# Optimization experiments

Hardware: AMD Instinct MI355X
Metric: run time of the kernel (lower is better)

Reference implementation:

```python
import jax, jax.numpy as jnp
import numpy as np

B, L, C = 8, 999, 768
C2 = C // 2           # 384 per branch
H, HD = 8, C2 // 8    # heads, head_dim=48
K, G = 3, 2           # dynamic conv kernel size, num_groups
DC_IN = C2 // 4       # DynamicConv1d proj inner (reduction_ratio default 4) = 96
PJ_IN = max(16, C // 8)  # mixer proj inner_dim = 96
SCALE = HD ** -0.5
EPS = 1e-5


def _gelu(x):
    return jax.nn.gelu(x, approximate=False)


def _c1x1(x, w, b):
    # pointwise conv1d: x (B,Cin,L), w (Cout,Cin), b (Cout,)
    return jnp.einsum('bcl,oc->bol', x, w) + b[None, :, None]


def _dw3(x, w, b):
    # depthwise conv1d k=3 pad=1: x (B,Ch,L), w (Ch,3), b (Ch,) or None
    Lx = x.shape[-1]
    xp = jnp.pad(x, ((0, 0), (0, 0), (1, 1)))
    y = (xp[:, :, 0:Lx] * w[:, 0][None, :, None]
         + xp[:, :, 1:Lx + 1] * w[:, 1][None, :, None]
         + xp[:, :, 2:Lx + 2] * w[:, 2][None, :, None])
    if b is not None:
        y = y + b[None, :, None]
    return y


def _bn(x, g, b):
    # BatchNorm1d, training-mode batch stats over (B, L): x (B,Ch,L)
    m = x.mean(axis=(0, 2), keepdims=True)
    v = ((x - m) ** 2).mean(axis=(0, 2), keepdims=True)
    return (x - m) * jax.lax.rsqrt(v + EPS) * g[None, :, None] + b[None, :, None]


def setup_inputs() -> dict:
    key = jax.random.key(0)
    ks = jax.random.split(key, 30)
    s = 0.02
    d = {
        'x': jax.random.normal(ks[0], (B, L, C), jnp.float32),
        # DynamicConv1d (dim=384, K=3, G=2, inner=96)
        'dc_weight': jax.random.normal(ks[1], (G, C2, K), jnp.float32) * s,
        'dc_bias':   jax.random.normal(ks[2], (G, C2), jnp.float32) * s,
        'dc_p1w':    jax.random.normal(ks[3], (DC_IN, C2), jnp.float32) * s,
        'dc_p1b':    jax.random.normal(ks[4], (DC_IN,), jnp.float32) * s,
        'dc_p2w':    jax.random.normal(ks[5], (C2 * G, DC_IN), jnp.float32) * s,
        'dc_p2b':    jax.random.normal(ks[6], (C2 * G,), jnp.float32) * s,
        # Attention (dim=384, heads=8, sr_ratio=1 -> sr=Identity)
        'at_qw':  jax.random.normal(ks[7], (C2, C2), jnp.float32) * s,
        'at_qb':  jax.random.normal(ks[8], (C2,), jnp.float32) * s,
        'at_kvw': jax.random.normal(ks[9], (2 * C2, C2), jnp.float32) * s,
        'at_kvb': jax.random.normal(ks[10], (2 * C2,), jnp.float32) * s,
        'at_lcw': jax.random.normal(ks[11], (C2, K), jnp.float32) * s,
        'at_lcb': jax.random.normal(ks[12], (C2,), jnp.float32) * s,
        # mixer proj
        'pj_dww':  jax.random.normal(ks[13], (C, K), jnp.float32) * s,
        'pj_dwb':  jax.random.normal(ks[14], (C,), jnp.float32) * s,
        'pj_bn1g': jnp.ones((C,), jnp.float32),
        'pj_bn1b': jnp.zeros((C,), jnp.float32),
        'pj_c1w':  jax.random.normal(ks[15], (PJ_IN, C), jnp.float32) * s,
        'pj_c1b':  jax.random.normal(ks[16], (PJ_IN,), jnp.float32) * s,
        'pj_bn2g': jnp.ones((PJ_IN,), jnp.float32),
        'pj_bn2b': jnp.zeros((PJ_IN,), jnp.float32),
        'pj_c2w':  jax.random.normal(ks[17], (C, PJ_IN), jnp.float32) * s,
        'pj_c2b':  jax.random.normal(ks[18], (C,), jnp.float32) * s,
        'pj_bn3g': jnp.ones((C,), jnp.float32),
        'pj_bn3b': jnp.zeros((C,), jnp.float32),
    }
    return d


def _dynamic_conv(x, dc_weight, dc_bias, p1w, p1b, p2w, p2b):
    # x: (B, L, C2)
    xt = jnp.transpose(x, (0, 2, 1))                 # (B,C2,L)
    # AdaptiveAvgPool1d(K) with L divisible by K -> exact non-overlapping mean
    pooled = xt.reshape(B, C2, K, L // K).mean(-1)   # (B,C2,K)
    sc = _c1x1(_gelu(_c1x1(pooled, p1w, p1b)), p2w, p2b)  # (B, G*C2, K)
    sc = jax.nn.softmax(sc.reshape(B, G, C2, K), axis=1)
    w = (sc * dc_weight[None]).sum(axis=1)           # (B,C2,K) per-sample kernels
    xm = xt.mean(axis=2, keepdims=True)              # (B,C2,1)
    sb = _c1x1(_gelu(_c1x1(xm, p1w, p1b)), p2w, p2b) # (B, G*C2, 1)
    sb = jax.nn.softmax(sb.reshape(B, G, C2), axis=1)
    bias = (sb * dc_bias[None]).sum(axis=1)          # (B,C2)
    # depthwise per-(b,c) conv, k=3, pad=1
    xp = jnp.pad(xt, ((0, 0), (0, 0), (1, 1)))
    y = (xp[:, :, 0:L] * w[:, :, 0:1]
         + xp[:, :, 1:L + 1] * w[:, :, 1:2]
         + xp[:, :, 2:L + 2] * w[:, :, 2:3]) + bias[:, :, None]
    return jnp.transpose(y, (0, 2, 1))               # (B,L,C2)


def _attention(x, qw, qb, kvw, kvb, lcw, lcb):
    # x: (B, L, C2)
    xt = jnp.transpose(x, (0, 2, 1))                 # (B,C2,L)
    q = _c1x1(xt, qw, qb).reshape(B, H, HD, L)
    q = jnp.transpose(q, (0, 1, 3, 2))               # (B,H,L,HD)
    kv_in = _dw3(xt, lcw, lcb) + xt                  # local_conv(kv)+kv (sr=Identity)
    kv = _c1x1(kv_in, kvw, kvb)                      # (B,2*C2,L)
    k = kv[:, :C2].reshape(B, H, HD, L)              # (B,H,HD,L)
    v = jnp.transpose(kv[:, C2:].reshape(B, H, HD, L), (0, 1, 3, 2))  # (B,H,L,HD)
    attn = jnp.einsum('bhld,bhdm->bhlm', q, k) * SCALE
    attn = jax.nn.softmax(attn, axis=-1)
    out = jnp.einsum('bhlm,bhmd->bhld', attn, v)     # (B,H,L,HD)
    # faithful to torch: transpose(-1,-2) then reshape(B, L, C2)
    out = jnp.transpose(out, (0, 1, 3, 2)).reshape(B, L, C2)
    return out


def reference(x, dc_weight, dc_bias, dc_p1w, dc_p1b, dc_p2w, dc_p2b,
              at_qw, at_qb, at_kvw, at_kvb, at_lcw, at_lcb,
              pj_dww, pj_dwb, pj_bn1g, pj_bn1b, pj_c1w, pj_c1b,
              pj_bn2g, pj_bn2b, pj_c2w, pj_c2b, pj_bn3g, pj_bn3b):
    x1 = x[:, :, :C2]
    x2 = x[:, :, C2:]
    x1 = _dynamic_conv(x1, dc_weight, dc_bias, dc_p1w, dc_p1b, dc_p2w, dc_p2b)
    x2 = _attention(x2, at_qw, at_qb, at_kvw, at_kvb, at_lcw, at_lcb)
    xc = jnp.concatenate([x1, x2], axis=2)           # (B,L,C)
    xt = jnp.transpose(xc, (0, 2, 1))                # (B,C,L)
    h = _bn(_gelu(_dw3(xt, pj_dww, pj_dwb)), pj_bn1g, pj_bn1b)
    h = _bn(_gelu(_c1x1(h, pj_c1w, pj_c1b)), pj_bn2g, pj_bn2b)
    h = _bn(_c1x1(h, pj_c2w, pj_c2b), pj_bn3g, pj_bn3b)
    out = h + xt
    return jnp.transpose(out, (0, 2, 1))             # (B,L,C)
```

## Files before the change

### kernel.cpp

```cpp
#include <hip/hip_runtime.h>
#include <cstddef>

constexpr int B = 8, L = 999, C = 768, C2 = 384, H = 8, HD = 48;
constexpr int KVL = 1000;
constexpr float ATT_SCALE = 0.14433756729740644f;
constexpr float LOG2E = 1.4426950408889634f;
constexpr float BN_EPS = 1e-5f;
constexpr float INV_N = 1.0f / (8.0f * 999.0f);

constexpr size_t SZ_XT   = (size_t)B * C * L;
constexpr size_t SZ_HALF = (size_t)B * C2 * L;
constexpr size_t OFF_XT  = 0;
constexpr size_t OFF_XT2 = SZ_XT;
constexpr size_t OFF_KV  = 2 * SZ_XT;
constexpr size_t OFF_AX  = 3 * SZ_XT;
constexpr size_t OFF_Q   = 3 * SZ_XT + SZ_HALF;
constexpr size_t OFF_SM  = 3 * SZ_XT + SZ_HALF + SZ_HALF / 2;

constexpr size_t SM_POOLED = 0;
constexpr size_t SM_XM     = 9216;
constexpr size_t SM_H1     = 12288;
constexpr size_t SM_WDYN   = 15360;
constexpr size_t SM_BDYN   = 24576;
constexpr size_t SM_SUM1   = 27648;
constexpr size_t SM_SQ1    = 28416;
constexpr size_t SM_S1     = 29184;
constexpr size_t SM_M1     = 29952;
constexpr size_t SM_CB1    = 30720;
constexpr size_t SM_SUM2   = 30816;
constexpr size_t SM_SQ2    = 30912;
constexpr size_t SM_S2     = 31008;
constexpr size_t SM_M2     = 31104;
constexpr size_t SM_CB2    = 31200;
constexpr size_t SM_SUM3   = 31968;
constexpr size_t SM_SQ3    = 32736;
constexpr size_t SM_S3     = 33504;
constexpr size_t SM_D3     = 34272;
constexpr size_t SM_END    = 35040;
constexpr size_t SM_WQ  = SM_END;
constexpr size_t SM_WKV = SM_WQ + 73728;
constexpr size_t SM_WC1 = SM_WKV + 147456;
constexpr size_t SM_WC2 = SM_WC1 + 36864;

typedef __attribute__((ext_vector_type(8))) short bf16x8;
typedef __attribute__((ext_vector_type(4))) float floatx4;

__device__ __forceinline__ float gelu_f(float x) {
  return 0.5f * x * (1.0f + erff(x * 0.70710678118654752f));
}

__device__ __forceinline__ float wave_sum(float v) {
  #pragma unroll
  for (int off = 32; off > 0; off >>= 1) v += __shfl_down(v, off, 64);
  return v;
}

__device__ __forceinline__ short f2bf(float f) {
  union { float f; unsigned u; } x; x.f = f;
  unsigned r = x.u + 0x7FFFu + ((x.u >> 16) & 1u);
  return (short)(r >> 16);
}

__device__ __forceinline__ bf16x8 pack8(const float* p) {
  union { unsigned u[4]; bf16x8 v; } r;
  asm("v_cvt_pk_bf16_f32 %0, %1, %2" : "=v"(r.u[0]) : "v"(p[0]), "v"(p[1]));
  asm("v_cvt_pk_bf16_f32 %0, %1, %2" : "=v"(r.u[1]) : "v"(p[2]), "v"(p[3]));
  asm("v_cvt_pk_bf16_f32 %0, %1, %2" : "=v"(r.u[2]) : "v"(p[4]), "v"(p[5]));
  asm("v_cvt_pk_bf16_f32 %0, %1, %2" : "=v"(r.u[3]) : "v"(p[6]), "v"(p[7]));
  return r.v;
}

__device__ __forceinline__ float exp2_hw(float x) {
  float r;
  asm("v_exp_f32 %0, %1" : "=v"(r) : "v"(x));
  return r;
}

__global__ void k_prep(const float* __restrict__ qw, short* __restrict__ wq,
                       const float* __restrict__ kvw, short* __restrict__ wkv,
                       const float* __restrict__ c1w, short* __restrict__ wc1,
                       const float* __restrict__ c2w, short* __restrict__ wc2,
                       const float* __restrict__ c1b, const float* __restrict__ bn1b,
                       const float* __restrict__ c2b, const float* __restrict__ bn2b,
                       float* __restrict__ cb1, float* __restrict__ cb2) {
  int bid = blockIdx.x;
  if (bid < 288) {
    const float* src; short* dst; int base;
    if (bid < 72)       { src = qw;  dst = wq;  base = bid; }
    else if (bid < 216) { src = kvw; dst = wkv; base = bid - 72; }
    else if (bid < 252) { src = c1w; dst = wc1; base = bid - 216; }
    else                { src = c2w; dst = wc2; base = bid - 252; }
    int i = (base * 256 + threadIdx.x) * 8;
    float4 a = *reinterpret_cast<const float4*>(&src[i]);
    float4 b = *reinterpret_cast<const float4*>(&src[i + 4]);
    short tmp[8] = {f2bf(a.x), f2bf(a.y), f2bf(a.z), f2bf(a.w),
                    f2bf(b.x), f2bf(b.y), f2bf(b.z), f2bf(b.w)};
    *(bf16x8*)&dst[i] = *(bf16x8*)tmp;
  } else if (bid == 288) {
    int o = threadIdx.x;
    if (o < 96) {
      float a = c1b[o];
      const float* wr = c1w + (size_t)o * C;
      for (int c = 0; c < C; c++) a += bn1b[c] * wr[c];
      cb1[o] = a;
    }
  } else {
    for (int o = threadIdx.x; o < C; o += 256) {
      float a = c2b[o];
      const float* wr = c2w + (size_t)o * 96;
      for (int i = 0; i < 96; i++) a += bn2b[i] * wr[i];
      cb2[o] = a;
    }
  }
}

__global__ __launch_bounds__(384) void k_kvin(const float* __restrict__ x,
                                              const float* __restrict__ lcw,
                                              const float* __restrict__ lcb,
                                              short* __restrict__ x2bf,
                                              short* __restrict__ kvinbf) {
  int b = blockIdx.y, l0 = blockIdx.x * 8, c = threadIdx.x;
  float w0 = lcw[c * 3], w1 = lcw[c * 3 + 1] + 1.0f, w2 = lcw[c * 3 + 2], bb = lcb[c];
  const float* xb = x + (size_t)b * L * C + C2 + c;
  float prev = (l0 > 0) ? xb[(size_t)(l0 - 1) * C] : 0.f;
  float cur  = (l0 < L) ? xb[(size_t)l0 * C] : 0.f;
  #pragma unroll
  for (int r = 0; r < 8; r++) {
    int l = l0 + r;
    if (l >= L) break;
    float nxt = (l + 1 < L) ? xb[(size_t)(l + 1) * C] : 0.f;
    x2bf[((size_t)b * L + l) * C2 + c]   = f2bf(cur);
    kvinbf[((size_t)b * L + l) * C2 + c] = f2bf(prev * w0 + cur * w1 + nxt * w2 + bb);
    prev = cur; cur = nxt;
  }
}

__global__ void k_transpose_in(const float* __restrict__ x, float* __restrict__ xt) {
  __shared__ float tile[32][33];
  int b = blockIdx.z;
  int l0 = blockIdx.x * 32, c0 = blockIdx.y * 32;
  int tx = threadIdx.x, ty = threadIdx.y;
  #pragma unroll
  for (int i = 0; i < 4; i++) {
    int l = l0 + ty + i * 8, c = c0 + tx;
    if (l < L) tile[ty + i * 8][tx] = x[((size_t)b * L + l) * C + c];
  }
  __syncthreads();
  #pragma unroll
  for (int i = 0; i < 4; i++) {
    int c = c0 + ty + i * 8, l = l0 + tx;
    if (l < L) xt[((size_t)b * C + c) * L + l] = tile[tx][ty + i * 8];
  }
}

__global__ __launch_bounds__(256) void k_pool(const float* __restrict__ xt,
                                              float* __restrict__ pooled,
                                              float* __restrict__ xm) {
  int c = blockIdx.x, b = blockIdx.y;
  const float* row = xt + ((size_t)b * C + c) * L;
  float s0 = 0.f, s1 = 0.f, s2 = 0.f;
  for (int l = threadIdx.x; l < L; l += 256) {
    float v = row[l];
    int ch = l / 333;
    if (ch == 0) s0 += v; else if (ch == 1) s1 += v; else s2 += v;
  }
  s0 = wave_sum(s0); s1 = wave_sum(s1); s2 = wave_sum(s2);
  __shared__ float r[3][4];
  int lane = threadIdx.x & 63, wid = threadIdx.x >> 6;
  if (lane == 0) { r[0][wid] = s0; r[1][wid] = s1; r[2][wid] = s2; }
  __syncthreads();
  if (threadIdx.x == 0) {
    float t0 = r[0][0] + r[0][1] + r[0][2] + r[0][3];
    float t1 = r[1][0] + r[1][1] + r[1][2] + r[1][3];
    float t2 = r[2][0] + r[2][1] + r[2][2] + r[2][3];
    size_t pb = (size_t)(b * C2 + c) * 3;
    pooled[pb + 0] = t0 / 333.f;
    pooled[pb + 1] = t1 / 333.f;
    pooled[pb + 2] = t2 / 333.f;
    xm[b * C2 + c] = (t0 + t1 + t2) / 999.f;
  }
}

__global__ void k_mlp1(const float* __restrict__ pooled, const float* __restrict__ xm,
                       const float* __restrict__ p1w, const float* __restrict__ p1b,
                       float* __restrict__ h1) {
  int j = blockIdx.x, b = blockIdx.y;
  __shared__ float vin[C2];
  for (int c = threadIdx.x; c < C2; c += 128)
    vin[c] = (j < 3) ? pooled[(size_t)(b * C2 + c) * 3 + j] : xm[b * C2 + c];
  __syncthreads();
  int o = threadIdx.x;
  if (o < 96) {
    float acc = p1b[o];
    const float* wr = p1w + (size_t)o * C2;
    for (int c = 0; c < C2; c++) acc += vin[c] * wr[c];
    h1[(b * 4 + j) * 96 + o] = gelu_f(acc);
  }
}

__global__ void k_mix2(const float* __restrict__ h1,
                       const float* __restrict__ p2w, const float* __restrict__ p2b,
                       const float* __restrict__ dcw, const float* __restrict__ dcb,
                       float* __restrict__ wdyn, float* __restrict__ bdyn) {
  int j = blockIdx.x, b = blockIdx.y;
  __shared__ float hv[96];
  for (int i = threadIdx.x; i < 96; i += 384) hv[i] = h1[(b * 4 + j) * 96 + i];
  __syncthreads();
  int c = threadIdx.x;
  float a0 = p2b[c], a1 = p2b[C2 + c];
  const float* w0r = p2w + (size_t)c * 96;
  const float* w1r = p2w + (size_t)(C2 + c) * 96;
  for (int i = 0; i < 96; i++) { float h = hv[i]; a0 += h * w0r[i]; a1 += h * w1r[i]; }
  float m = fmaxf(a0, a1);
  float e0 = __expf(a0 - m), e1 = __expf(a1 - m);
  float inv = 1.f / (e0 + e1);
  float p0 = e0 * inv, p1 = e1 * inv;
  if (j < 3)
    wdyn[(size_t)(b * C2 + c) * 3 + j] = p0 * dcw[(size_t)c * 3 + j] + p1 * dcw[(size_t)(C2 + c) * 3 + j];
  else
    bdyn[b * C2 + c] = p0 * dcb[c] + p1 * dcb[C2 + c];
}

__global__ __launch_bounds__(256) void k_dwconv(const float* __restrict__ xt,
                                                const float* __restrict__ wdyn,
                                                const float* __restrict__ bdyn,
                                                float* __restrict__ xt2) {
  int c = blockIdx.x, b = blockIdx.y;
  const float* rowA = xt + ((size_t)b * C + c) * L;
  size_t wb = (size_t)(b * C2 + c) * 3;
  float a0 = wdyn[wb], a1 = wdyn[wb + 1], a2 = wdyn[wb + 2], ab = bdyn[b * C2 + c];
  float* oA = xt2 + ((size_t)b * C + c) * L;
  for (int l = threadIdx.x; l < L; l += 256) {
    float xm1 = (l > 0) ? rowA[l - 1] : 0.f;
    float x0 = rowA[l];
    float xp1 = (l < L - 1) ? rowA[l + 1] : 0.f;
    oA[l] = xm1 * a0 + x0 * a1 + xp1 * a2 + ab;
  }
}

template<int LT, bool XBF16>
__global__ __launch_bounds__(256) void k_gemm3(const short* __restrict__ Wbf,
                                               const void* __restrict__ Xv,
                                               void* __restrict__ Yv,
                                               const float* __restrict__ shift,
                                               const float* __restrict__ scale,
                                               const float* __restrict__ bias,
                                               float* __restrict__ sum, float* __restrict__ sq,
                                               int O, int Kd, int Kstride, int XLd, int Ldy,
                                               size_t xbs, size_t ybs,
                                               int flags, float outmul,
                                               int ksplit, size_t slice) {
  __shared__ __align__(16) short Xt[2][LT * 72];
  constexpr int R = LT / 32;
  int b = blockIdx.z;
  int kc = (int)blockIdx.y % ksplit;
  int o0 = ((int)blockIdx.y / ksplit) * 64;
  int l0 = blockIdx.x * LT;
  int kbeg = kc * Kd;
  int t = threadIdx.x, w = t >> 6, lane = t & 63;
  int col = lane & 15, quad = lane >> 4;
  int KT = (Kd + 63) >> 6;

  floatx4 acc[LT / 16];
  #pragma unroll
  for (int i = 0; i < LT / 16; i++) acc[i] = floatx4{0.f, 0.f, 0.f, 0.f};

  int orow = o0 + w * 16 + col;
  bool wok = orow < O;
  const short* Wrow = Wbf + (size_t)orow * Kstride + kbeg;

  const short* Xb16 = (const short*)Xv + (size_t)b * xbs + kbeg;
  const float* Xb32 = (const float*)Xv + (size_t)b * xbs + kbeg;

  bf16x8 xr[R];
  float4 xf[R][2];
  bf16x8 wcur0, wcur1, wnxt0, wnxt1;

  auto xload = [&](int k0) {
    #pragma unroll
    for (int r = 0; r < R; r++) {
      int u = t + r * 256;
      int ll = u >> 3, oct = u & 7;
      int l = l0 + ll, kk = k0 + oct * 8;
      bool ok = (l < L) && (kk < Kd);
      if constexpr (XBF16) {
        xr[r] = ok ? *(const bf16x8*)&Xb16[(size_t)l * XLd + kk]
                   : bf16x8{0, 0, 0, 0, 0, 0, 0, 0};
      } else {
        if (ok) {
          const float* p = &Xb32[(size_t)l * XLd + kk];
          float4 a = *(const float4*)p;
          float4 bq = *(const float4*)(p + 4);
          if (shift) {
            float4 sh0 = *(const float4*)&shift[kbeg + kk];
            float4 sh1 = *(const float4*)&shift[kbeg + kk + 4];
            float4 sc0 = *(const float4*)&scale[kbeg + kk];
            float4 sc1 = *(const float4*)&scale[kbeg + kk + 4];
            a.x = (a.x - sh0.x) * sc0.x;  a.y = (a.y - sh0.y) * sc0.y;
            a.z = (a.z - sh0.z) * sc0.z;  a.w = (a.w - sh0.w) * sc0.w;
            bq.x = (bq.x - sh1.x) * sc1.x; bq.y = (bq.y - sh1.y) * sc1.y;
            bq.z = (bq.z - sh1.z) * sc1.z; bq.w = (bq.w - sh1.w) * sc1.w;
          }
          xf[r][0] = a;
          xf[r][1] = bq;
        } else {
          xf[r][0] = float4{0.f, 0.f, 0.f, 0.f};
          xf[r][1] = float4{0.f, 0.f, 0.f, 0.f};
        }
      }
    }
  };
  auto xwrite = [&](int buf) {
    #pragma unroll
    for (int r = 0; r < R; r++) {
      int u = t + r * 256;
      int ll = u >> 3, oct = u & 7;
      bf16x8 val;
      if constexpr (XBF16) {
        val = xr[r];
      } else {
        union { unsigned u4[4]; bf16x8 v; } pk;
        asm("v_cvt_pk_bf16_f32 %0, %1, %2" : "=v"(pk.u4[0]) : "v"(xf[r][0].x), "v"(xf[r][0].y));
        asm("v_cvt_pk_bf16_f32 %0, %1, %2" : "=v"(pk.u4[1]) : "v"(xf[r][0].z), "v"(xf[r][0].w));
        asm("v_cvt_pk_bf16_f32 %0, %1, %2" : "=v"(pk.u4[2]) : "v"(xf[r][1].x), "v"(xf[r][1].y));
        asm("v_cvt_pk_bf16_f32 %0, %1, %2" : "=v"(pk.u4[3]) : "v"(xf[r][1].z), "v"(xf[r][1].w));
        val = pk.v;
      }
      *(bf16x8*)&Xt[buf][ll * 72 + oct * 8] = val;
    }
  };
  auto wload = [&](int k0, bf16x8& f0, bf16x8& f1) {
    int kk0 = k0 + quad * 8;
    int kk1 = k0 + 32 + quad * 8;
    f0 = (wok && kk0 < Kd) ? *(const bf16x8*)&Wrow[kk0] : bf16x8{0, 0, 0, 0, 0, 0, 0, 0};
    f1 = (wok && kk1 < Kd) ? *(const bf16x8*)&Wrow[kk1] : bf16x8{0, 0, 0, 0, 0, 0, 0, 0};
  };

  xload(0);
  wload(0, wcur0, wcur1);
  xwrite(0);
  __syncthreads();

  for (int it = 0; it < KT; ++it) {
    int curb = it & 1;
    bool more = (it + 1 < KT);
    if (more) { xload((it + 1) * 64); wload((it + 1) * 64, wnxt0, wnxt1); }
    #pragma unroll
    for (int nt = 0; nt < LT / 16; nt++) {
      bf16x8 bx0 = *(bf16x8*)&Xt[curb][(nt * 16 + col) * 72 + quad * 8];
      acc[nt] = __builtin_amdgcn_mfma_f32_16x16x32_bf16(wcur0, bx0, acc[nt], 0, 0, 0);
      bf16x8 bx1 = *(bf16x8*)&Xt[curb][(nt * 16 + col) * 72 + 32 + quad * 8];
      acc[nt] = __builtin_amdgcn_mfma_f32_16x16x32_bf16(wcur1, bx1, acc[nt], 0, 0, 0);
    }
    if (more) xwrite(curb ^ 1);
    __syncthreads();
    wcur0 = wnxt0; wcur1 = wnxt1;
  }

  int o_base = o0 + w * 16 + quad * 4;
  #pragma unroll
  for (int r = 0; r < 4; r++) {
    int o = o_base + r;
    bool ov = o < O;
    float bo = (bias && ov) ? bias[o] : 0.f;
    float ps = 0.f, pq = 0.f;
    #pragma unroll
    for (int nt = 0; nt < LT / 16; nt++) {
      int l = l0 + nt * 16 + col;
      float v = acc[nt][r] + bo;
      if (flags & 1) v = gelu_f(v);
      v *= outmul;
      if (l >= L) v = 0.f;
      if (ov && l < L) {
        if (flags & 2) ((short*)Yv)[(size_t)b * ybs + (size_t)o * Ldy + l] = f2bf(v);
        else           ((float*)Yv)[kc * slice + (size_t)b * ybs + (size_t)o * Ldy + l] = v;
      }
      ps += v; pq += v * v;
    }
    if ((flags & 8) && ov) {
      ps += __shfl_xor(ps, 1); ps += __shfl_xor(ps, 2);
      ps += __shfl_xor(ps, 4); ps += __shfl_xor(ps, 8);
      pq += __shfl_xor(pq, 1); pq += __shfl_xor(pq, 2);
      pq += __shfl_xor(pq, 4); pq += __shfl_xor(pq, 8);
      if (col == 0) { atomicAdd(&sum[o], ps); atomicAdd(&sq[o], pq); }
    }
  }
}

__global__ __launch_bounds__(256) void k_h2fin_t(const float* __restrict__ part,
                                                 const float* __restrict__ cb1,
                                                 float* __restrict__ h2,
                                                 float* __restrict__ sum, float* __restrict__ sq) {
  __shared__ float tile[96][33];
  __shared__ float lsum[96], lsq[96];
  constexpr size_t SL = (size_t)B * 96 * L;
  int b = blockIdx.y, l0 = blockIdx.x * 32;
  int t = threadIdx.x;
  #pragma unroll
  for (int p = 0; p < 12; p++) {
    int u = t + p * 256;
    int o = u >> 5, li = u & 31;
    int l = l0 + li;
    float v = 0.f;
    if (l < L) {
      size_t idx = ((size_t)b * 96 + o) * L + l;
      v = gelu_f(part[idx] + part[SL + idx] + part[2 * SL + idx] + part[3 * SL + idx] + cb1[o]);
    }
    tile[o][li] = v;
    float vs = v, vq = v * v;
    vs += __shfl_xor(vs, 1); vs += __shfl_xor(vs, 2); vs += __shfl_xor(vs, 4);
    vs += __shfl_xor(vs, 8); vs += __shfl_xor(vs, 16);
    vq += __shfl_xor(vq, 1); vq += __shfl_xor(vq, 2); vq += __shfl_xor(vq, 4);
    vq += __shfl_xor(vq, 8); vq += __shfl_xor(vq, 16);
    if ((t & 31) == 0) { lsum[o] = vs; lsq[o] = vq; }
  }
  __syncthreads();
  if (t < 96) { atomicAdd(&sum[t], lsum[t]); atomicAdd(&sq[t], lsq[t]); }
  #pragma unroll
  for (int p = 0; p < 12; p++) {
    int u = t + p * 256;
    int lr = u / 96, o = u % 96;
    int l = l0 + lr;
    if (l < L) h2[((size_t)b * L + l) * 96 + o] = tile[o][lr];
  }
}

__global__ __launch_bounds__(512, 4) void k_attn_mfma(const short* __restrict__ q,
                                                      const short* __restrict__ kv,
                                                      float* __restrict__ out) {
  __shared__ __align__(16) char smem[2 * 8192 + 2 * 6144 + 33280];
  short* Ks0 = (short*)smem;
  short* Ks1 = (short*)(smem + 8192);
  short* Vf0 = (short*)(smem + 16384);
  short* Vf1 = (short*)(smem + 22528);
  float* PF  = (float*)(smem + 28672);
  float* Os  = (float*)smem;

  int lt0 = blockIdx.x * 128;
  int h = blockIdx.y, b = blockIdx.z;
  int t = threadIdx.x;
  int w = t >> 6, lane = t & 63;
  int col = lane & 15, quad = lane >> 4;
  const short* qb = q  + ((size_t)b * C2 + h * HD) * L;
  const short* kb = kv + ((size_t)b * C  + h * HD) * KVL;
  const short* vb = kv + ((size_t)b * C + C2 + h * HD) * KVL;

  bf16x8 aq0, aq1;
  {
    int l = lt0 + w * 16 + col;
    bool ok = l < L;
    const short* qp = qb + (size_t)(quad * 8) * L + l;
    short v0[8];
    #pragma unroll
    for (int jj = 0; jj < 8; jj++) v0[jj] = ok ? qp[(size_t)jj * L] : (short)0;
    aq0 = *(bf16x8*)v0;
    if (quad < 2) {
      const short* qp1 = qb + (size_t)(32 + quad * 8) * L + l;
      short v1[8];
      #pragma unroll
      for (int jj = 0; jj < 8; jj++) v1[jj] = ok ? qp1[(size_t)jj * L] : (short)0;
      aq1 = *(bf16x8*)v1;
    } else {
      aq1 = bf16x8{0, 0, 0, 0, 0, 0, 0, 0};
    }
  }

  short kreg[8];
  bf16x8 vreg;

  auto stage_load = [&](int m0) {
    if (t < 384) {
      int m = t & 63, j = t >> 6;
      int gm = m0 + m;
      bool ok = gm < L;
      const short* src = kb + (size_t)(8 * j) * KVL + gm;
      #pragma unroll
      for (int jj = 0; jj < 8; jj++) kreg[jj] = ok ? src[(size_t)jj * KVL] : (short)0;
    }
    if (t >= 128) {
      int a = t - 128;
      int d = (a & 7) | ((a >> 6) << 3);
      int o = (a >> 3) & 7;
      int mb = m0 + o * 8;
      const short* src = vb + (size_t)d * KVL + mb;
      if (mb + 8 <= L) {
        vreg = *(const bf16x8*)src;
      } else {
        short tmp[8];
        #pragma unroll
        for (int j = 0; j < 8; j++) tmp[j] = (mb + j < L) ? src[j] : (short)0;
        vreg = *(bf16x8*)tmp;
      }
    }
  };
  auto stage_write = [&](short* Kd, short* Vd) {
    if (t < 384) {
      int m = t & 63, j = t >> 6;
      int slot = ((m >> 4) * 2 + (j >> 2)) * 64 + (j & 3) * 16 + (m & 15);
      *(bf16x8*)&Kd[slot * 8] = *(bf16x8*)kreg;
    }
    if (t >= 128) {
      int a = t - 128;
      int d = (a & 7) | ((a >> 6) << 3);
      int o = (a >> 3) & 7;
      int lanep = ((o & 3) << 4) | (d & 15);
      *(bf16x8*)&Vd[(((o >> 2) * 3 + (d >> 4)) * 64 + lanep) * 8] = vreg;
    }
  };

  if (t < 256) {
    int i = t & 127;
    int ms = i >> 5, qq = 2 + ((i >> 4) & 1), cc = i & 15;
    int slot = (ms * 2 + 1) * 64 + qq * 16 + cc;
    short* Kd = (t < 128) ? Ks0 : Ks1;
    *(bf16x8*)&Kd[slot * 8] = bf16x8{0, 0, 0, 0, 0, 0, 0, 0};
  }

  stage_load(0);
  stage_write(Ks0, Vf0);

  floatx4 of[3];
  #pragma unroll
  for (int i = 0; i < 3; i++) of[i] = floatx4{0.f, 0.f, 0.f, 0.f};
  float rs[4] = {0.f, 0.f, 0.f, 0.f};
  __syncthreads();

  for (int it = 0; it < 16; ++it) {
    int m0 = it * 64;
    short* Kc = (it & 1) ? Ks1 : Ks0;
    short* Vc = (it & 1) ? Vf1 : Vf0;
    short* Kn = (it & 1) ? Ks0 : Ks1;
    short* Vn = (it & 1) ? Vf0 : Vf1;
    if (it < 15) stage_load(m0 + 64);

    floatx4 sf[4];
    __builtin_amdgcn_s_setprio(1);
    #pragma unroll
    for (int ms = 0; ms < 4; ms++) {
      bf16x8 bk0 = *(bf16x8*)&Kc[((ms * 2 + 0) * 64 + lane) * 8];
      bf16x8 bk1 = *(bf16x8*)&Kc[((ms * 2 + 1) * 64 + lane) * 8];
      floatx4 a4 = floatx4{0.f, 0.f, 0.f, 0.f};
      a4 = __builtin_amdgcn_mfma_f32_16x16x32_bf16(aq0, bk0, a4, 0, 0, 0);
      a4 = __builtin_amdgcn_mfma_f32_16x16x32_bf16(aq1, bk1, a4, 0, 0, 0);
      sf[ms] = a4;
    }
    __builtin_amdgcn_s_setprio(0);

    float* pw = PF + w * 1040 + lane;
    #pragma unroll
    for (int ms = 0; ms < 4; ms++) {
      int m = m0 + ms * 16 + col;
      bool ok = m < L;
      #pragma unroll
      for (int r = 0; r < 4; r++) {
        float e = ok ? exp2_hw(sf[ms][r]) : 0.f;
        rs[r] += e;
        pw[(ms * 4 + r) * 65] = e;
      }
    }

    const float* pr = PF + w * 1040 + (col & 3) * 65 + (col >> 2) * 16 + (quad & 1) * 8;
    __builtin_amdgcn_s_setprio(1);
    #pragma unroll
    for (int mh = 0; mh < 2; mh++) {
      const float* ps = pr + (mh * 2 + (quad >> 1)) * 260;
      float p8[8];
      #pragma unroll
      for (int jj = 0; jj < 8; jj++) p8[jj] = ps[jj];
      bf16x8 ap = pack8(p8);
      #pragma unroll
      for (int ds = 0; ds < 3; ds++) {
        bf16x8 bv = *(bf16x8*)&Vc[((mh * 3 + ds) * 64 + lane) * 8];
        of[ds] = __builtin_amdgcn_mfma_f32_16x16x32_bf16(ap, bv, of[ds], 0, 0, 0);
      }
    }
    __builtin_amdgcn_s_setprio(0);
    if (it < 15) stage_write(Kn, Vn);
    __syncthreads();
  }

  #pragma unroll
  for (int r = 0; r < 4; r++) {
    float v = rs[r];
    v += __shfl_xor(v, 1); v += __shfl_xor(v, 2);
    v += __shfl_xor(v, 4); v += __shfl_xor(v, 8);
    rs[r] = v;
  }
  #pragma unroll
  for (int r = 0; r < 4; r++) {
    float inv = 1.f / rs[r];
    #pragma unroll
    for (int ds = 0; ds < 3; ds++)
      Os[(ds * 16 + col) * 130 + w * 16 + quad * 4 + r] = of[ds][r] * inv;
  }
  __syncthreads();
  for (int i = t; i < 48 * 128; i += 512) {
    int d = i >> 7, ll = i & 127;
    int l = lt0 + ll;
    if (l < L) out[((size_t)b * C2 + h * HD + d) * L + l] = Os[d * 130 + ll];
  }
}

__global__ void k_fill_xt2(const float* __restrict__ ao, float* __restrict__ xt2) {
  __shared__ float tile[32][33];
  int b = blockIdx.z;
  int l0 = blockIdx.x * 32, c0 = blockIdx.y * 32;
  int tx = threadIdx.x, ty = threadIdx.y;
  #pragma unroll
  for (int i = 0; i < 4; i++) {
    int l = l0 + ty + i * 8, c = c0 + tx;
    if (l < L) tile[ty + i * 8][tx] = ao[(size_t)b * ((size_t)L * C2) + (size_t)l * C2 + c];
  }
  __syncthreads();
  #pragma unroll
  for (int i = 0; i < 4; i++) {
    int c = c0 + ty + i * 8, l = l0 + tx;
    if (l < L) xt2[((size_t)b * C + C2 + c) * L + l] = tile[tx][ty + i * 8];
  }
}

__global__ __launch_bounds__(256) void k_dwproj_t(const float* __restrict__ xt2,
                                                  const float* __restrict__ dww,
                                                  const float* __restrict__ dwb,
                                                  float* __restrict__ t1,
                                                  float* __restrict__ sum, float* __restrict__ sq) {
  __shared__ float tile[32][67];
  __shared__ float rs[4][32], rq[4][32];
  int b = blockIdx.z, c0 = blockIdx.y * 32, l0 = blockIdx.x * 64;
  int t = threadIdx.x;
  for (int u = t; u < 32 * 66; u += 256) {
    int cc = u / 66, li = u % 66;
    int l = l0 - 1 + li;
    tile[cc][li] = (l >= 0 && l < L) ? xt2[((size_t)b * C + c0 + cc) * L + l] : 0.f;
  }
  __syncthreads();
  int c = c0 + (t & 31);
  float w0 = dww[c * 3], w1 = dww[c * 3 + 1], w2 = dww[c * 3 + 2], bb = dwb[c];
  int cc = t & 31;
  float s = 0.f, s2 = 0.f;
  #pragma unroll
  for (int p = 0; p < 8; p++) {
    int lr = (t >> 5) + p * 8;
    int l = l0 + lr;
    float v = 0.f;
    if (l < L) {
      v = gelu_f(tile[cc][lr] * w0 + tile[cc][lr + 1] * w1 + tile[cc][lr + 2] * w2 + bb);
      t1[((size_t)b * L + l) * C + c] = v;
    }
    s += v; s2 += v * v;
  }
  s += __shfl_xor(s, 32, 64); s2 += __shfl_xor(s2, 32, 64);
  int wv = t >> 6, ln = t & 63;
  if (ln < 32) { rs[wv][ln] = s; rq[wv][ln] = s2; }
  __syncthreads();
  if (t < 32) {
    float a = rs[0][t] + rs[1][t] + rs[2][t] + rs[3][t];
    float qq = rq[0][t] + rq[1][t] + rq[2][t] + rq[3][t];
    atomicAdd(&sum[c0 + t], a);
    atomicAdd(&sq[c0 + t], qq);
  }
}

__global__ void k_bnfin(const float* __restrict__ sum, const float* __restrict__ sq,
                        const float* __restrict__ g, int n,
                        float* __restrict__ s_, float* __restrict__ m_) {
  int t = threadIdx.x;
  if (t < n) {
    float m = sum[t] * INV_N;
    float v = sq[t] * INV_N - m * m;
    float r = rsqrtf(v + BN_EPS);
    s_[t] = g[t] * r;
    m_[t] = m;
  }
}

__global__ void k_fin3(const float* __restrict__ sum, const float* __restrict__ sq,
                       const float* __restrict__ g, const float* __restrict__ be,
                       float* __restrict__ s3, float* __restrict__ d3) {
  int t = threadIdx.x;
  if (t < C) {
    float m = sum[t] * INV_N;
    float v = sq[t] * INV_N - m * m;
    float r = rsqrtf(v + BN_EPS);
    float sc = g[t] * r;
    s3[t] = sc;
    d3[t] = be[t] - m * sc;
  }
}

__global__ void k_final(const float* __restrict__ y3, const float* __restrict__ xt2,
                        const float* __restrict__ s3, const float* __restrict__ d3,
                        float* __restrict__ out) {
  __shared__ float tile[32][33];
  int b = blockIdx.z;
  int l0 = blockIdx.x * 32, c0 = blockIdx.y * 32;
  int tx = threadIdx.x, ty = threadIdx.y;
  #pragma unroll
  for (int i = 0; i < 4; i++) {
    int c = c0 + ty + i * 8, l = l0 + tx;
    if (l < L) {
      size_t idx = ((size_t)b * C + c) * L + l;
      tile[ty + i * 8][tx] = y3[idx] * s3[c] + d3[c] + xt2[idx];
    }
  }
  __syncthreads();
  #pragma unroll
  for (int i = 0; i < 4; i++) {
    int l = l0 + ty + i * 8, c = c0 + tx;
    if (l < L) out[((size_t)b * L + l) * C + c] = tile[tx][ty + i * 8];
  }
}

extern "C" void kernel_launch(void* const* d_in, const int* in_sizes, int n_in,
                              void* d_out, int out_size, void* d_ws, size_t ws_size,
                              hipStream_t stream) {
  const float* x    = (const float*)d_in[0];
  const float* dcw  = (const float*)d_in[1];
  const float* dcb  = (const float*)d_in[2];
  const float* p1w  = (const float*)d_in[3];
  const float* p1b  = (const float*)d_in[4];
  const float* p2w  = (const float*)d_in[5];
  const float* p2b  = (const float*)d_in[6];
  const float* qw   = (const float*)d_in[7];
  const float* qb   = (const float*)d_in[8];
  const float* kvw  = (const float*)d_in[9];
  const float* kvb  = (const float*)d_in[10];
  const float* lcw  = (const float*)d_in[11];
  const float* lcb  = (const float*)d_in[12];
  const float* dww  = (const float*)d_in[13];
  const float* dwb  = (const float*)d_in[14];
  const float* bn1g = (const float*)d_in[15];
  const float* bn1b = (const float*)d_in[16];
  const float* c1w  = (const float*)d_in[17];
  const float* c1b  = (const float*)d_in[18];
  const float* bn2g = (const float*)d_in[19];
  const float* bn2b = (const float*)d_in[20];
  const float* c2w  = (const float*)d_in[21];
  const float* c2b  = (const float*)d_in[22];
  const float* bn3g = (const float*)d_in[23];
  const float* bn3b = (const float*)d_in[24];
  float* out = (float*)d_out;
  float* ws  = (float*)d_ws;

  float* xt      = ws + OFF_XT;
  float* xt2     = ws + OFF_XT2;
  short* kvbuf   = (short*)(ws + OFF_KV);
  float* y3      = ws + OFF_KV;
  short* x2bf    = (short*)(ws + OFF_AX);
  short* kvinbf  = (short*)(ws + OFF_AX + SZ_HALF / 2);
  float* attnout = ws + OFF_AX;
  float* c1part  = ws + OFF_AX;
  short* qbuf    = (short*)(ws + OFF_Q);
  float* h2      = ws + OFF_Q;
  float* sm      = ws + OFF_SM;

  float* pooled = sm + SM_POOLED;
  float* xm     = sm + SM_XM;
  float* h1     = sm + SM_H1;
  float* wdyn   = sm + SM_WDYN;
  float* bdyn   = sm + SM_BDYN;
  float* sum1 = sm + SM_SUM1; float* sq1 = sm + SM_SQ1;
  float* s1 = sm + SM_S1; float* m1 = sm + SM_M1; float* cb1 = sm + SM_CB1;
  float* sum2 = sm + SM_SUM2; float* sq2 = sm + SM_SQ2;
  float* s2 = sm + SM_S2; float* m2 = sm + SM_M2; float* cb2 = sm + SM_CB2;
  float* sum3 = sm + SM_SUM3; float* sq3 = sm + SM_SQ3;
  float* s3 = sm + SM_S3; float* d3 = sm + SM_D3;
  short* wqbf  = (short*)(sm + SM_WQ);
  short* wkvbf = (short*)(sm + SM_WKV);
  short* wc1bf = (short*)(sm + SM_WC1);
  short* wc2bf = (short*)(sm + SM_WC2);

  hipMemsetAsync((void*)(sm + SM_SUM1), 0, (SM_S3 - SM_SUM1) * sizeof(float), stream);

  k_prep<<<290, 256, 0, stream>>>(qw, wqbf, kvw, wkvbf, c1w, wc1bf, c2w, wc2bf,
                                  c1b, bn1b, c2b, bn2b, cb1, cb2);
  k_kvin<<<dim3(125, B), 384, 0, stream>>>(x, lcw, lcb, x2bf, kvinbf);

  dim3 tb32(32, 8);
  k_transpose_in<<<dim3(32, 12, B), tb32, 0, stream>>>(x, xt);
  k_pool<<<dim3(C2, B), 256, 0, stream>>>(xt, pooled, xm);
  k_mlp1<<<dim3(4, B), 128, 0, stream>>>(pooled, xm, p1w, p1b, h1);
  k_mix2<<<dim3(4, B), 384, 0, stream>>>(h1, p2w, p2b, dcw, dcb, wdyn, bdyn);
  k_dwconv<<<dim3(C2, B), 256, 0, stream>>>(xt, wdyn, bdyn, xt2);
  k_gemm3<64, true><<<dim3(16, 6, B), 256, 0, stream>>>(
      wqbf, (const void*)x2bf, (void*)qbuf, nullptr, nullptr, qb, nullptr, nullptr,
      C2, C2, C2, C2, L, (size_t)C2 * L, (size_t)C2 * L, 2, ATT_SCALE * LOG2E, 1, 0);
  k_gemm3<128, true><<<dim3(8, 12, B), 256, 0, stream>>>(
      wkvbf, (const void*)kvinbf, (void*)kvbuf, nullptr, nullptr, kvb, nullptr, nullptr,
      C, C2, C2, C2, KVL, (size_t)C2 * L, (size_t)C * KVL, 2, 1.0f, 1, 0);
  k_attn_mfma<<<dim3(8, H, B), 512, 0, stream>>>(qbuf, kvbuf, attnout);
  k_fill_xt2<<<dim3(32, 12, B), tb32, 0, stream>>>(attnout, xt2);
  k_dwproj_t<<<dim3(16, 24, B), 256, 0, stream>>>(xt2, dww, dwb, xt, sum1, sq1);
  k_bnfin<<<1, 768, 0, stream>>>(sum1, sq1, bn1g, C, s1, m1);
  k_gemm3<128, false><<<dim3(8, 8, B), 256, 0, stream>>>(
      wc1bf, (const void*)xt, (void*)c1part, m1, s1, nullptr, nullptr, nullptr,
      96, 192, C, C, L, (size_t)C * L, (size_t)96 * L, 0, 1.0f, 4, (size_t)B * 96 * L);
  k_h2fin_t<<<dim3(32, B), 256, 0, stream>>>(c1part, cb1, h2, sum2, sq2);
  k_bnfin<<<1, 768, 0, stream>>>(sum2, sq2, bn2g, 96, s2, m2);
  k_gemm3<128, false><<<dim3(8, 12, B), 256, 0, stream>>>(
      wc2bf, (const void*)h2, (void*)y3, m2, s2, cb2, sum3, sq3,
      C, 96, 96, 96, L, (size_t)96 * L, (size_t)C * L, 8, 1.0f, 1, 0);
  k_fin3<<<1, 768, 0, stream>>>(sum3, sq3, bn3g, bn3b, s3, d3);
  k_final<<<dim3(32, 24, B), tb32, 0, stream>>>(y3, xt2, s3, d3, out);
}
```

Before: 354.7 us.

## Fuse small kernels: merge Q/KV GEMMs, inline BN finalize, drop transpose passes

Merges the input transpose into the weight-prep kernel and the Q and KV projection GEMMs into one launch. It deletes the BN-finalize kernels by computing mean and scale from the sums inside the consuming GEMM loaders and the final kernel. It also removes the attention-output transpose into xt2, so the depthwise-projection and final kernels read the attention output directly in (B,L,C2) layout. Together these cut launch count and one full transpose round trip through memory. The cost is redundant rsqrt and BN math per element in the GEMM X-loads and the final kernel, a strided gather for half the channels in the dwproj tile load, and a larger 128-wide L tile for the Q GEMM.

```diff
diff --git a/kernel.cpp b/kernel.cpp
--- a/kernel.cpp
+++ b/kernel.cpp
@@ -24,18 +24,13 @@
 constexpr size_t SM_BDYN   = 24576;
 constexpr size_t SM_SUM1   = 27648;
 constexpr size_t SM_SQ1    = 28416;
-constexpr size_t SM_S1     = 29184;
-constexpr size_t SM_M1     = 29952;
 constexpr size_t SM_CB1    = 30720;
 constexpr size_t SM_SUM2   = 30816;
 constexpr size_t SM_SQ2    = 30912;
-constexpr size_t SM_S2     = 31008;
-constexpr size_t SM_M2     = 31104;
 constexpr size_t SM_CB2    = 31200;
 constexpr size_t SM_SUM3   = 31968;
 constexpr size_t SM_SQ3    = 32736;
-constexpr size_t SM_S3     = 33504;
-constexpr size_t SM_D3     = 34272;
+constexpr size_t SM_ZEND   = 33504;
 constexpr size_t SM_END    = 35040;
 constexpr size_t SM_WQ  = SM_END;
 constexpr size_t SM_WKV = SM_WQ + 73728;
@@ -76,40 +71,61 @@
   return r;
 }
 
-__global__ void k_prep(const float* __restrict__ qw, short* __restrict__ wq,
-                       const float* __restrict__ kvw, short* __restrict__ wkv,
-                       const float* __restrict__ c1w, short* __restrict__ wc1,
-                       const float* __restrict__ c2w, short* __restrict__ wc2,
-                       const float* __restrict__ c1b, const float* __restrict__ bn1b,
-                       const float* __restrict__ c2b, const float* __restrict__ bn2b,
-                       float* __restrict__ cb1, float* __restrict__ cb2) {
+#define BNA(x, su, qq, gg) { float m_ = (su) * INV_N; float v_ = (qq) * INV_N - m_ * m_; \
+  float sc_ = (gg) * rsqrtf(v_ + BN_EPS); (x) = ((x) - m_) * sc_; }
+
+__global__ void k_pre_t(const float* __restrict__ qw, short* __restrict__ wq,
+                        const float* __restrict__ kvw, short* __restrict__ wkv,
+                        const float* __restrict__ c1w, short* __restrict__ wc1,
+                        const float* __restrict__ c2w, short* __restrict__ wc2,
+                        const float* __restrict__ c1b, const float* __restrict__ bn1b,
+                        const float* __restrict__ c2b, const float* __restrict__ bn2b,
+                        float* __restrict__ cb1, float* __restrict__ cb2,
+                        const float* __restrict__ x, float* __restrict__ xt) {
+  __shared__ float tile[32][33];
   int bid = blockIdx.x;
+  int t = threadIdx.y * 32 + threadIdx.x;
   if (bid < 288) {
     const float* src; short* dst; int base;
     if (bid < 72)       { src = qw;  dst = wq;  base = bid; }
     else if (bid < 216) { src = kvw; dst = wkv; base = bid - 72; }
     else if (bid < 252) { src = c1w; dst = wc1; base = bid - 216; }
     else                { src = c2w; dst = wc2; base = bid - 252; }
-    int i = (base * 256 + threadIdx.x) * 8;
+    int i = (base * 256 + t) * 8;
     float4 a = *reinterpret_cast<const float4*>(&src[i]);
     float4 b = *reinterpret_cast<const float4*>(&src[i + 4]);
     short tmp[8] = {f2bf(a.x), f2bf(a.y), f2bf(a.z), f2bf(a.w),
                     f2bf(b.x), f2bf(b.y), f2bf(b.z), f2bf(b.w)};
     *(bf16x8*)&dst[i] = *(bf16x8*)tmp;
   } else if (bid == 288) {
-    int o = threadIdx.x;
-    if (o < 96) {
-      float a = c1b[o];
-      const float* wr = c1w + (size_t)o * C;
+    if (t < 96) {
+      float a = c1b[t];
+      const float* wr = c1w + (size_t)t * C;
       for (int c = 0; c < C; c++) a += bn1b[c] * wr[c];
-      cb1[o] = a;
-    }
-  } else {
-    for (int o = threadIdx.x; o < C; o += 256) {
+      cb1[t] = a;
+    }
+  } else if (bid == 289) {
+    for (int o = t; o < C; o += 256) {
       float a = c2b[o];
       const float* wr = c2w + (size_t)o * 96;
       for (int i = 0; i < 96; i++) a += bn2b[i] * wr[i];
       cb2[o] = a;
+    }
+  } else {
+    int tb = bid - 290;
+    int bx = tb % 32, by = (tb / 32) % 12, bz = tb / 384;
+    int l0 = bx * 32, c0 = by * 32;
+    int tx = threadIdx.x, ty = threadIdx.y;
+    #pragma unroll
+    for (int i = 0; i < 4; i++) {
+      int l = l0 + ty + i * 8, c = c0 + tx;
+      if (l < L) tile[ty + i * 8][tx] = x[((size_t)bz * L + l) * C + c];
+    }
+    __syncthreads();
+    #pragma unroll
+    for (int i = 0; i < 4; i++) {
+      int c = c0 + ty + i * 8, l = l0 + tx;
+      if (l < L) xt[((size_t)bz * C + c) * L + l] = tile[tx][ty + i * 8];
     }
   }
 }
@@ -132,24 +148,6 @@
     x2bf[((size_t)b * L + l) * C2 + c]   = f2bf(cur);
     kvinbf[((size_t)b * L + l) * C2 + c] = f2bf(prev * w0 + cur * w1 + nxt * w2 + bb);
     prev = cur; cur = nxt;
-  }
-}
-
-__global__ void k_transpose_in(const float* __restrict__ x, float* __restrict__ xt) {
-  __shared__ float tile[32][33];
-  int b = blockIdx.z;
-  int l0 = blockIdx.x * 32, c0 = blockIdx.y * 32;
-  int tx = threadIdx.x, ty = threadIdx.y;
-  #pragma unroll
-  for (int i = 0; i < 4; i++) {
-    int l = l0 + ty + i * 8, c = c0 + tx;
-    if (l < L) tile[ty + i * 8][tx] = x[((size_t)b * L + l) * C + c];
-  }
-  __syncthreads();
-  #pragma unroll
-  for (int i = 0; i < 4; i++) {
-    int c = c0 + ty + i * 8, l = l0 + tx;
-    if (l < L) xt[((size_t)b * C + c) * L + l] = tile[tx][ty + i * 8];
   }
 }
 
@@ -239,23 +237,22 @@
 }
 
 template<int LT, bool XBF16>
-__global__ __launch_bounds__(256) void k_gemm3(const short* __restrict__ Wbf,
-                                               const void* __restrict__ Xv,
-                                               void* __restrict__ Yv,
-                                               const float* __restrict__ shift,
-                                               const float* __restrict__ scale,
-                                               const float* __restrict__ bias,
-                                               float* __restrict__ sum, float* __restrict__ sq,
-                                               int O, int Kd, int Kstride, int XLd, int Ldy,
-                                               size_t xbs, size_t ybs,
-                                               int flags, float outmul,
-                                               int ksplit, size_t slice) {
-  __shared__ __align__(16) short Xt[2][LT * 72];
+__device__ __forceinline__ void gemm_body(const short* __restrict__ Wbf,
+                                          const void* __restrict__ Xv,
+                                          void* __restrict__ Yv,
+                                          const float* __restrict__ ssum,
+                                          const float* __restrict__ ssq,
+                                          const float* __restrict__ sg,
+                                          const float* __restrict__ bias,
+                                          float* __restrict__ osum, float* __restrict__ osq,
+                                          int O, int Kd, int Kstride, int XLd, int Ldy,
+                                          size_t xbs, size_t ybs,
+                                          int flags, float outmul,
+                                          int kc, size_t slice,
+                                          int o0, int l0, int b,
+                                          short* Xt) {
   constexpr int R = LT / 32;
-  int b = blockIdx.z;
-  int kc = (int)blockIdx.y % ksplit;
-  int o0 = ((int)blockIdx.y / ksplit) * 64;
-  int l0 = blockIdx.x * LT;
+  constexpr int XSZ = LT * 72;
   int kbeg = kc * Kd;
   int t = threadIdx.x, w = t >> 6, lane = t & 63;
   int col = lane & 15, quad = lane >> 4;
@@ -291,15 +288,17 @@
           const float* p = &Xb32[(size_t)l * XLd + kk];
           float4 a = *(const float4*)p;
           float4 bq = *(const float4*)(p + 4);
-          if (shift) {
-            float4 sh0 = *(const float4*)&shift[kbeg + kk];
-            float4 sh1 = *(const float4*)&shift[kbeg + kk + 4];
-            float4 sc0 = *(const float4*)&scale[kbeg + kk];
-            float4 sc1 = *(const float4*)&scale[kbeg + kk + 4];
-            a.x = (a.x - sh0.x) * sc0.x;  a.y = (a.y - sh0.y) * sc0.y;
-            a.z = (a.z - sh0.z) * sc0.z;  a.w = (a.w - sh0.w) * sc0.w;
-            bq.x = (bq.x - sh1.x) * sc1.x; bq.y = (bq.y - sh1.y) * sc1.y;
-            bq.z = (bq.z - sh1.z) * sc1.z; bq.w = (bq.w - sh1.w) * sc1.w;
+          if (sg) {
+            float4 u0 = *(const float4*)&ssum[kbeg + kk];
+            float4 u1 = *(const float4*)&ssum[kbeg + kk + 4];
+            float4 q0 = *(const float4*)&ssq[kbeg + kk];
+            float4 q1 = *(const float4*)&ssq[kbeg + kk + 4];
+            float4 g0 = *(const float4*)&sg[kbeg + kk];
+            float4 g1 = *(const float4*)&sg[kbeg + kk + 4];
+            BNA(a.x, u0.x, q0.x, g0.x);  BNA(a.y, u0.y, q0.y, g0.y);
+            BNA(a.z, u0.z, q0.z, g0.z);  BNA(a.w, u0.w, q0.w, g0.w);
+            BNA(bq.x, u1.x, q1.x, g1.x); BNA(bq.y, u1.y, q1.y, g1.y);
+            BNA(bq.z, u1.z, q1.z, g1.z); BNA(bq.w, u1.w, q1.w, g1.w);
           }
           xf[r][0] = a;
           xf[r][1] = bq;
@@ -326,7 +325,7 @@
         asm("v_cvt_pk_bf16_f32 %0, %1, %2" : "=v"(pk.u4[3]) : "v"(xf[r][1].z), "v"(xf[r][1].w));
         val = pk.v;
       }
-      *(bf16x8*)&Xt[buf][ll * 72 + oct * 8] = val;
+      *(bf16x8*)&Xt[buf * XSZ + ll * 72 + oct * 8] = val;
     }
   };
   auto wload = [&](int k0, bf16x8& f0, bf16x8& f1) {
@@ -347,9 +346,9 @@
     if (more) { xload((it + 1) * 64); wload((it + 1) * 64, wnxt0, wnxt1); }
     #pragma unroll
     for (int nt = 0; nt < LT / 16; nt++) {
-      bf16x8 bx0 = *(bf16x8*)&Xt[curb][(nt * 16 + col) * 72 + quad * 8];
+      bf16x8 bx0 = *(bf16x8*)&Xt[curb * XSZ + (nt * 16 + col) * 72 + quad * 8];
       acc[nt] = __builtin_amdgcn_mfma_f32_16x16x32_bf16(wcur0, bx0, acc[nt], 0, 0, 0);
-      bf16x8 bx1 = *(bf16x8*)&Xt[curb][(nt * 16 + col) * 72 + 32 + quad * 8];
+      bf16x8 bx1 = *(bf16x8*)&Xt[curb * XSZ + (nt * 16 + col) * 72 + 32 + quad * 8];
       acc[nt] = __builtin_amdgcn_mfma_f32_16x16x32_bf16(wcur1, bx1, acc[nt], 0, 0, 0);
     }
     if (more) xwrite(curb ^ 1);
@@ -382,8 +381,54 @@
       ps += __shfl_xor(ps, 4); ps += __shfl_xor(ps, 8);
       pq += __shfl_xor(pq, 1); pq += __shfl_xor(pq, 2);
       pq += __shfl_xor(pq, 4); pq += __shfl_xor(pq, 8);
-      if (col == 0) { atomicAdd(&sum[o], ps); atomicAdd(&sq[o], pq); }
-    }
+      if (col == 0) { atomicAdd(&osum[o], ps); atomicAdd(&osq[o], pq); }
+    }
+  }
+}
+
+template<int LT, bool XBF16>
+__global__ __launch_bounds__(256) void k_gemm3(const short* __restrict__ Wbf,
+                                               const void* __restrict__ Xv,
+                                               void* __restrict__ Yv,
+                                               const float* __restrict__ ssum,
+                                               const float* __restrict__ ssq,
+                                               const float* __restrict__ sg,
+                                               const float* __restrict__ bias,
+                                               float* __restrict__ osum, float* __restrict__ osq,
+                                               int O, int Kd, int Kstride, int XLd, int Ldy,
+                                               size_t xbs, size_t ybs,
+                                               int flags, float outmul,
+                                               int ksplit, size_t slice) {
+  __shared__ __align__(16) short Xt[2][LT * 72];
+  int kc = (int)blockIdx.y % ksplit;
+  int o0 = ((int)blockIdx.y / ksplit) * 64;
+  gemm_body<LT, XBF16>(Wbf, Xv, Yv, ssum, ssq, sg, bias, osum, osq,
+                       O, Kd, Kstride, XLd, Ldy, xbs, ybs, flags, outmul,
+                       kc, slice, o0, blockIdx.x * LT, blockIdx.z, &Xt[0][0]);
+}
+
+__global__ __launch_bounds__(256) void k_gemm_qkv(const short* __restrict__ wq,
+                                                  const short* __restrict__ wkv,
+                                                  const short* __restrict__ x2,
+                                                  const short* __restrict__ kvin,
+                                                  short* __restrict__ qout,
+                                                  short* __restrict__ kvout,
+                                                  const float* __restrict__ qbias,
+                                                  const float* __restrict__ kvbias) {
+  __shared__ __align__(16) short Xt[2][128 * 72];
+  int y = blockIdx.y;
+  if (y < 6) {
+    gemm_body<128, true>(wq, (const void*)x2, (void*)qout,
+                         nullptr, nullptr, nullptr, qbias, nullptr, nullptr,
+                         C2, C2, C2, C2, L, (size_t)C2 * L, (size_t)C2 * L,
+                         2, ATT_SCALE * LOG2E, 0, 0,
+                         y * 64, blockIdx.x * 128, blockIdx.z, &Xt[0][0]);
+  } else {
+    gemm_body<128, true>(wkv, (const void*)kvin, (void*)kvout,
+                         nullptr, nullptr, nullptr, kvbias, nullptr, nullptr,
+                         C, C2, C2, C2, KVL, (size_t)C2 * L, (size_t)C * KVL,
+                         2, 1.0f, 0, 0,
+                         (y - 6) * 64, blockIdx.x * 128, blockIdx.z, &Xt[0][0]);
   }
 }
 
@@ -601,25 +646,8 @@
   }
 }
 
-__global__ void k_fill_xt2(const float* __restrict__ ao, float* __restrict__ xt2) {
-  __shared__ float tile[32][33];
-  int b = blockIdx.z;
-  int l0 = blockIdx.x * 32, c0 = blockIdx.y * 32;
-  int tx = threadIdx.x, ty = threadIdx.y;
-  #pragma unroll
-  for (int i = 0; i < 4; i++) {
-    int l = l0 + ty + i * 8, c = c0 + tx;
-    if (l < L) tile[ty + i * 8][tx] = ao[(size_t)b * ((size_t)L * C2) + (size_t)l * C2 + c];
-  }
-  __syncthreads();
-  #pragma unroll
-  for (int i = 0; i < 4; i++) {
-    int c = c0 + ty + i * 8, l = l0 + tx;
-    if (l < L) xt2[((size_t)b * C + C2 + c) * L + l] = tile[tx][ty + i * 8];
-  }
-}
-
 __global__ __launch_bounds__(256) void k_dwproj_t(const float* __restrict__ xt2,
+                                                  const float* __restrict__ ao,
                                                   const float* __restrict__ dww,
                                                   const float* __restrict__ dwb,
                                                   float* __restrict__ t1,
@@ -628,10 +656,18 @@
   __shared__ float rs[4][32], rq[4][32];
   int b = blockIdx.z, c0 = blockIdx.y * 32, l0 = blockIdx.x * 64;
   int t = threadIdx.x;
-  for (int u = t; u < 32 * 66; u += 256) {
-    int cc = u / 66, li = u % 66;
-    int l = l0 - 1 + li;
-    tile[cc][li] = (l >= 0 && l < L) ? xt2[((size_t)b * C + c0 + cc) * L + l] : 0.f;
+  if (c0 < C2) {
+    for (int u = t; u < 32 * 66; u += 256) {
+      int cc = u / 66, li = u % 66;
+      int l = l0 - 1 + li;
+      tile[cc][li] = (l >= 0 && l < L) ? xt2[((size_t)b * C + c0 + cc) * L + l] : 0.f;
+    }
+  } else {
+    for (int u = t; u < 32 * 66; u += 256) {
+      int li = u >> 5, cc = u & 31;
+      int l = l0 - 1 + li;
+      tile[cc][li] = (l >= 0 && l < L) ? ao[((size_t)b * L + l) * C2 + (c0 - C2 + cc)] : 0.f;
+    }
   }
   __syncthreads();
   int c = c0 + (t & 31);
@@ -661,35 +697,10 @@
   }
 }
 
-__global__ void k_bnfin(const float* __restrict__ sum, const float* __restrict__ sq,
-                        const float* __restrict__ g, int n,
-                        float* __restrict__ s_, float* __restrict__ m_) {
-  int t = threadIdx.x;
-  if (t < n) {
-    float m = sum[t] * INV_N;
-    float v = sq[t] * INV_N - m * m;
-    float r = rsqrtf(v + BN_EPS);
-    s_[t] = g[t] * r;
-    m_[t] = m;
-  }
-}
-
-__global__ void k_fin3(const float* __restrict__ sum, const float* __restrict__ sq,
-                       const float* __restrict__ g, const float* __restrict__ be,
-                       float* __restrict__ s3, float* __restrict__ d3) {
-  int t = threadIdx.x;
-  if (t < C) {
-    float m = sum[t] * INV_N;
-    float v = sq[t] * INV_N - m * m;
-    float r = rsqrtf(v + BN_EPS);
-    float sc = g[t] * r;
-    s3[t] = sc;
-    d3[t] = be[t] - m * sc;
-  }
-}
-
 __global__ void k_final(const float* __restrict__ y3, const float* __restrict__ xt2,
-                        const float* __restrict__ s3, const float* __restrict__ d3,
+                        const float* __restrict__ ao,
+                        const float* __restrict__ sum3, const float* __restrict__ sq3,
+                        const float* __restrict__ bn3g, const float* __restrict__ bn3b,
                         float* __restrict__ out) {
   __shared__ float tile[32][33];
   int b = blockIdx.z;
@@ -699,15 +710,25 @@
   for (int i = 0; i < 4; i++) {
     int c = c0 + ty + i * 8, l = l0 + tx;
     if (l < L) {
+      float m = sum3[c] * INV_N;
+      float v = sq3[c] * INV_N - m * m;
+      float sc = bn3g[c] * rsqrtf(v + BN_EPS);
+      float dd = bn3b[c] - m * sc;
       size_t idx = ((size_t)b * C + c) * L + l;
-      tile[ty + i * 8][tx] = y3[idx] * s3[c] + d3[c] + xt2[idx];
+      float val = y3[idx] * sc + dd;
+      if (c < C2) val += xt2[idx];
+      tile[ty + i * 8][tx] = val;
     }
   }
   __syncthreads();
   #pragma unroll
   for (int i = 0; i < 4; i++) {
     int l = l0 + ty + i * 8, c = c0 + tx;
-    if (l < L) out[((size_t)b * L + l) * C + c] = tile[tx][ty + i * 8];
+    if (l < L) {
+      float val = tile[tx][ty + i * 8];
+      if (c >= C2) val += ao[((size_t)b * L + l) * C2 + (c - C2)];
+      out[((size_t)b * L + l) * C + c] = val;
+    }
   }
 }
 
@@ -745,11 +766,11 @@
   float* xt      = ws + OFF_XT;
   float* xt2     = ws + OFF_XT2;
   short* kvbuf   = (short*)(ws + OFF_KV);
+  float* c1part  = ws + OFF_KV;
   float* y3      = ws + OFF_KV;
   short* x2bf    = (short*)(ws + OFF_AX);
   short* kvinbf  = (short*)(ws + OFF_AX + SZ_HALF / 2);
   float* attnout = ws + OFF_AX;
-  float* c1part  = ws + OFF_AX;
   short* qbuf    = (short*)(ws + OFF_Q);
   float* h2      = ws + OFF_Q;
   float* sm      = ws + OFF_SM;
@@ -760,46 +781,35 @@
   float* wdyn   = sm + SM_WDYN;
   float* bdyn   = sm + SM_BDYN;
   float* sum1 = sm + SM_SUM1; float* sq1 = sm + SM_SQ1;
-  float* s1 = sm + SM_S1; float* m1 = sm + SM_M1; float* cb1 = sm + SM_CB1;
+  float* cb1 = sm + SM_CB1;
   float* sum2 = sm + SM_SUM2; float* sq2 = sm + SM_SQ2;
-  float* s2 = sm + SM_S2; float* m2 = sm + SM_M2; float* cb2 = sm + SM_CB2;
+  float* cb2 = sm + SM_CB2;
   float* sum3 = sm + SM_SUM3; float* sq3 = sm + SM_SQ3;
-  float* s3 = sm + SM_S3; float* d3 = sm + SM_D3;
   short* wqbf  = (short*)(sm + SM_WQ);
   short* wkvbf = (short*)(sm + SM_WKV);
   short* wc1bf = (short*)(sm + SM_WC1);
   short* wc2bf = (short*)(sm + SM_WC2);
 
-  hipMemsetAsync((void*)(sm + SM_SUM1), 0, (SM_S3 - SM_SUM1) * sizeof(float), stream);
-
-  k_prep<<<290, 256, 0, stream>>>(qw, wqbf, kvw, wkvbf, c1w, wc1bf, c2w, wc2bf,
-                                  c1b, bn1b, c2b, bn2b, cb1, cb2);
+  hipMemsetAsync((void*)(sm + SM_SUM1), 0, (SM_ZEND - SM_SUM1) * sizeof(float), stream);
+
+  dim3 tb32(32, 8);
+  k_pre_t<<<3362, tb32, 0, stream>>>(qw, wqbf, kvw, wkvbf, c1w, wc1bf, c2w, wc2bf,
+                                     c1b, bn1b, c2b, bn2b, cb1, cb2, x, xt);
   k_kvin<<<dim3(125, B), 384, 0, stream>>>(x, lcw, lcb, x2bf, kvinbf);
-
-  dim3 tb32(32, 8);
-  k_transpose_in<<<dim3(32, 12, B), tb32, 0, stream>>>(x, xt);
   k_pool<<<dim3(C2, B), 256, 0, stream>>>(xt, pooled, xm);
   k_mlp1<<<dim3(4, B), 128, 0, stream>>>(pooled, xm, p1w, p1b, h1);
   k_mix2<<<dim3(4, B), 384, 0, stream>>>(h1, p2w, p2b, dcw, dcb, wdyn, bdyn);
   k_dwconv<<<dim3(C2, B), 256, 0, stream>>>(xt, wdyn, bdyn, xt2);
-  k_gemm3<64, true><<<dim3(16, 6, B), 256, 0, stream>>>(
-      wqbf, (const void*)x2bf, (void*)qbuf, nullptr, nullptr, qb, nullptr, nullptr,
-      C2, C2, C2, C2, L, (size_t)C2 * L, (size_t)C2 * L, 2, ATT_SCALE * LOG2E, 1, 0);
-  k_gemm3<128, true><<<dim3(8, 12, B), 256, 0, stream>>>(
-      wkvbf, (const void*)kvinbf, (void*)kvbuf, nullptr, nullptr, kvb, nullptr, nullptr,
-      C, C2, C2, C2, KVL, (size_t)C2 * L, (size_t)C * KVL, 2, 1.0f, 1, 0);
+  k_gemm_qkv<<<dim3(8, 18, B), 256, 0, stream>>>(wqbf, wkvbf, x2bf, kvinbf,
+                                                 qbuf, kvbuf, qb, kvb);
   k_attn_mfma<<<dim3(8, H, B), 512, 0, stream>>>(qbuf, kvbuf, attnout);
-  k_fill_xt2<<<dim3(32, 12, B), tb32, 0, stream>>>(attnout, xt2);
-  k_dwproj_t<<<dim3(16, 24, B), 256, 0, stream>>>(xt2, dww, dwb, xt, sum1, sq1);
-  k_bnfin<<<1, 768, 0, stream>>>(sum1, sq1, bn1g, C, s1, m1);
+  k_dwproj_t<<<dim3(16, 24, B), 256, 0, stream>>>(xt2, attnout, dww, dwb, xt, sum1, sq1);
   k_gemm3<128, false><<<dim3(8, 8, B), 256, 0, stream>>>(
-      wc1bf, (const void*)xt, (void*)c1part, m1, s1, nullptr, nullptr, nullptr,
+      wc1bf, (const void*)xt, (void*)c1part, sum1, sq1, bn1g, nullptr, nullptr, nullptr,
       96, 192, C, C, L, (size_t)C * L, (size_t)96 * L, 0, 1.0f, 4, (size_t)B * 96 * L);
   k_h2fin_t<<<dim3(32, B), 256, 0, stream>>>(c1part, cb1, h2, sum2, sq2);
-  k_bnfin<<<1, 768, 0, stream>>>(sum2, sq2, bn2g, 96, s2, m2);
   k_gemm3<128, false><<<dim3(8, 12, B), 256, 0, stream>>>(
-      wc2bf, (const void*)h2, (void*)y3, m2, s2, cb2, sum3, sq3,
+      wc2bf, (const void*)h2, (void*)y3, sum2, sq2, bn2g, cb2, sum3, sq3,
       C, 96, 96, 96, L, (size_t)96 * L, (size_t)C * L, 8, 1.0f, 1, 0);
-  k_fin3<<<1, 768, 0, stream>>>(sum3, sq3, bn3g, bn3b, s3, d3);
-  k_final<<<dim3(32, 24, B), tb32, 0, stream>>>(y3, xt2, s3, d3, out);
-}
+  k_final<<<dim3(32, 24, B), tb32, 0, stream>>>(y3, xt2, attnout, sum3, sq3, bn3g, bn3b, out);
+}
```

Result: faster. 326.5 us (-7.9%).
